# Kernel tuning notes

Measured on AMD Instinct MI355X. Metric: run time of the kernel, lower is better.

## Reference

```python
import jax, jax.numpy as jnp
import numpy as np

VOCAB, EMBED, HIDDEN = 256, 512, 1024
B, T = 64, 512


def setup_inputs() -> dict:
    key = jax.random.key(0)
    ks = jax.random.split(key, 12)
    s = 0.02
    return {
        "x": jax.random.randint(ks[0], (B, T), 0, VOCAB),
        "embed": jax.random.normal(ks[1], (VOCAB, EMBED), jnp.float32) * s,
        "Wih0": jax.random.normal(ks[2], (3 * HIDDEN, EMBED), jnp.float32) * s,
        "Whh0": jax.random.normal(ks[3], (3 * HIDDEN, HIDDEN), jnp.float32) * s,
        "bih0": jax.random.normal(ks[4], (3 * HIDDEN,), jnp.float32) * s,
        "bhh0": jax.random.normal(ks[5], (3 * HIDDEN,), jnp.float32) * s,
        "Wih1": jax.random.normal(ks[6], (3 * HIDDEN, HIDDEN), jnp.float32) * s,
        "Whh1": jax.random.normal(ks[7], (3 * HIDDEN, HIDDEN), jnp.float32) * s,
        "bih1": jax.random.normal(ks[8], (3 * HIDDEN,), jnp.float32) * s,
        "bhh1": jax.random.normal(ks[9], (3 * HIDDEN,), jnp.float32) * s,
        "W_out": jax.random.normal(ks[10], (VOCAB, HIDDEN), jnp.float32) * s,
        "b_out": jax.random.normal(ks[11], (VOCAB,), jnp.float32) * s,
    }


def gru_cell(inp, h, Wih, Whh, bih, bhh):
    # PyTorch GRUCell math.
    gi = inp @ Wih.T + bih  # (B, 3H)
    gh = h @ Whh.T + bhh    # (B, 3H)
    i_r, i_z, i_n = jnp.split(gi, 3, axis=-1)
    h_r, h_z, h_n = jnp.split(gh, 3, axis=-1)
    r = jax.nn.sigmoid(i_r + h_r)
    z = jax.nn.sigmoid(i_z + h_z)
    n = jnp.tanh(i_n + r * h_n)
    return (1.0 - z) * n + z * h


def reference(x, embed, Wih0, Whh0, bih0, bhh0, Wih1, Whh1, bih1, bhh1, W_out, b_out):
    emb = embed[x]                       # (B, T, E)
    xs = jnp.swapaxes(emb, 0, 1)         # (T, B, E)
    h0 = jnp.zeros((x.shape[0], HIDDEN), emb.dtype)

    def step(carry, inp_t):
        h_0, h_1 = carry
        h_0 = gru_cell(inp_t, h_0, Wih0, Whh0, bih0, bhh0)
        h_1 = gru_cell(h_0, h_1, Wih1, Whh1, bih1, bhh1)
        return (h_0, h_1), h_1

    _, outs = jax.lax.scan(step, (h0, h0), xs)   # outs: (T, B, H)
    outs = jnp.swapaxes(outs, 0, 1)              # (B, T, H)
    logits = outs @ W_out.T + b_out              # (B, T, V)
    return logits
```

## Files before the change

kernel.cpp:

```cpp
#include <hip/hip_runtime.h>
#include <stdint.h>

typedef short short8 __attribute__((ext_vector_type(8)));
typedef float f32x4 __attribute__((ext_vector_type(4)));
typedef unsigned short u16;

#define MFMA16(a, b, c) __builtin_amdgcn_mfma_f32_16x16x32_bf16((a), (b), (c), 0, 0, 0)

#define T_LEN 512
#define BATCH 64
#define EMB_D 512
#define HID 1024
#define VOC 256
#define NWG 128
#define RNN_THREADS 512

#define OFF_H0B   1048576u
#define OFF_H1B   1310720u
#define HB_ZERO_BYTES 524288u
#define OFF_EMB   1573120u
#define OFF_WIH0  (OFF_EMB + 33554432u)
#define OFF_WHH0  (OFF_WIH0 + 3145728u)
#define OFF_WIH1  (OFF_WHH0 + 6291456u)
#define OFF_WHH1  (OFF_WIH1 + 6291456u)
#define OFF_WOUT  (OFF_WHH1 + 6291456u)
#define OFF_H1ALL (OFF_WOUT + 524288u)
#define OFF_SYNC  (OFF_H1ALL + 67108864u)
#define SYNC_BYTES 16640u
#define WS_TOTAL  (OFF_SYNC + SYNC_BYTES)

static __device__ __forceinline__ u16 f2b(float f) {
  uint32_t u = __float_as_uint(f);
  u += 0x7FFFu + ((u >> 16) & 1u);
  return (u16)(u >> 16);
}
static __device__ __forceinline__ float sigm(float x) { return 1.0f / (1.0f + __expf(-x)); }

__global__ void cvt_kernel(const float* __restrict__ src, u16* __restrict__ dst, int n) {
  int i = ((int)blockIdx.x * 256 + (int)threadIdx.x) * 4;
  if (i + 4 <= n) {
    const float4 v = *(const float4*)(src + i);
    ushort4 o;
    o.x = f2b(v.x); o.y = f2b(v.y); o.z = f2b(v.z); o.w = f2b(v.w);
    *(ushort4*)(dst + i) = o;
  }
}

__global__ void emb_kernel(const int* __restrict__ x, const float* __restrict__ embed,
                           u16* __restrict__ emb_all) {
  const int r = (int)blockIdx.x * 4 + ((int)threadIdx.x >> 6);
  const int c = ((int)threadIdx.x & 63) * 8;
  const int t = r >> 6, b = r & 63;
  const int xi = x[b * T_LEN + t];
  const float* s = embed + (size_t)xi * EMB_D + c;
  const float4 v0 = *(const float4*)s;
  const float4 v1 = *(const float4*)(s + 4);
  ushort4 lo, hi;
  lo.x = f2b(v0.x); lo.y = f2b(v0.y); lo.z = f2b(v0.z); lo.w = f2b(v0.w);
  hi.x = f2b(v1.x); hi.y = f2b(v1.y); hi.z = f2b(v1.z); hi.w = f2b(v1.w);
  u16* d = emb_all + (size_t)r * EMB_D + c;
  *(ushort4*)d = lo;
  *(ushort4*)(d + 4) = hi;
}

__global__ __launch_bounds__(RNN_THREADS, 1) void rnn_persist_kernel(
    const u16* __restrict__ emb_all,
    const u16* __restrict__ A0i_r, const u16* __restrict__ A0i_z, const u16* __restrict__ A0i_n,
    const u16* __restrict__ A0h_r, const u16* __restrict__ A0h_z, const u16* __restrict__ A0h_n,
    const u16* __restrict__ A1i_r, const u16* __restrict__ A1i_z, const u16* __restrict__ A1i_n,
    const u16* __restrict__ A1h_r, const u16* __restrict__ A1h_z, const u16* __restrict__ A1h_n,
    const float* __restrict__ bih0, const float* __restrict__ bhh0,
    const float* __restrict__ bih1, const float* __restrict__ bhh1,
    u16* __restrict__ h0b, u16* __restrict__ h1b,
    u16* __restrict__ h1all, unsigned* __restrict__ flags)
{
  __shared__ __align__(16) float lds[16384];
  const int tid = (int)threadIdx.x;
  const int wv = tid >> 6;
  const int lane = tid & 63;
  const int lrow = lane & 15;
  const int lk8 = (lane >> 4) << 3;
  const int wgid = (int)blockIdx.x;
  const int layer = wgid >> 6;
  const int ubase = (wgid & 63) << 4;
  const bool iwave = (wv < 4);
  const bool l0i = (layer == 0) && iwave;

  const u16 *Ar, *Az, *An;
  int ldb, k0;
  if (layer == 0) {
    if (iwave) { Ar = A0i_r; Az = A0i_z; An = A0i_n; ldb = EMB_D; k0 = wv * 128; }
    else       { Ar = A0h_r; Az = A0h_z; An = A0h_n; ldb = HID;   k0 = (wv - 4) * 256; }
  } else {
    if (iwave) { Ar = A1i_r; Az = A1i_z; An = A1i_n; ldb = HID;   k0 = wv * 256; }
    else       { Ar = A1h_r; Az = A1h_z; An = A1h_n; ldb = HID;   k0 = (wv - 4) * 256; }
  }
  const size_t arow = (size_t)(ubase + lrow) * ldb;

  short8 a4R[4], a4Z[4], a4N[4];
  short8 a8R[8], a8Z[8], a8N[8];
  if (l0i) {
#pragma unroll
    for (int ks = 0; ks < 4; ++ks) {
      const int kk = k0 + ks * 32 + lk8;
      a4R[ks] = *(const short8*)(Ar + arow + kk);
      a4Z[ks] = *(const short8*)(Az + arow + kk);
      a4N[ks] = *(const short8*)(An + arow + kk);
    }
  } else {
#pragma unroll
    for (int ks = 0; ks < 8; ++ks) {
      const int kk = k0 + ks * 32 + lk8;
      a8R[ks] = *(const short8*)(Ar + arow + kk);
      a8Z[ks] = *(const short8*)(Az + arow + kk);
      a8N[ks] = *(const short8*)(An + arow + kk);
    }
  }

  const float* bi = layer ? bih1 : bih0;
  const float* bh = layer ? bhh1 : bhh0;
  const int eu = tid & 15;
  const int eug = ubase + eu;
  const float bR = bi[eug] + bh[eug];
  const float bZ = bi[HID + eug] + bh[HID + eug];
  const float bNi = bi[2 * HID + eug];
  const float bNh = bh[2 * HID + eug];
  const int el = ((eu >> 2) << 4);
  const int er = eu & 3;
  u16* hb = layer ? h1b : h0b;
  float hprev[2] = {0.f, 0.f};

  for (int s = 0; s <= T_LEN; ++s) {
    const bool active = (layer == 0) ? (s < T_LEN) : (s >= 1);
    if (active) {
      const int rdA = ((s + 1) & 1) * (BATCH * HID);
      const u16* Bp;
      if (layer == 0) Bp = iwave ? (emb_all + (size_t)s * (BATCH * EMB_D)) : (h0b + rdA);
      else            Bp = iwave ? (h0b + rdA) : (h1b + (s & 1) * (BATCH * HID));

      f32x4 acc0[4], acc1[4], accn[4];
#pragma unroll
      for (int bt = 0; bt < 4; ++bt) {
        acc0[bt] = (f32x4){0.f, 0.f, 0.f, 0.f};
        acc1[bt] = (f32x4){0.f, 0.f, 0.f, 0.f};
        accn[bt] = (f32x4){0.f, 0.f, 0.f, 0.f};
      }
      if (l0i) {
#pragma unroll
        for (int ks = 0; ks < 4; ++ks) {
          const int kk = k0 + ks * 32 + lk8;
#pragma unroll
          for (int bt = 0; bt < 4; ++bt) {
            const short8 bf = *(const short8*)(Bp + (size_t)(bt * 16 + lrow) * EMB_D + kk);
            acc0[bt] = MFMA16(a4R[ks], bf, acc0[bt]);
            acc1[bt] = MFMA16(a4Z[ks], bf, acc1[bt]);
            accn[bt] = MFMA16(a4N[ks], bf, accn[bt]);
          }
        }
      } else {
#pragma unroll
        for (int ks = 0; ks < 8; ++ks) {
          const int kk = k0 + ks * 32 + lk8;
#pragma unroll
          for (int bt = 0; bt < 4; ++bt) {
            const short8 bf = *(const short8*)(Bp + (size_t)(bt * 16 + lrow) * HID + kk);
            acc0[bt] = MFMA16(a8R[ks], bf, acc0[bt]);
            acc1[bt] = MFMA16(a8Z[ks], bf, acc1[bt]);
            accn[bt] = MFMA16(a8N[ks], bf, accn[bt]);
          }
        }
      }
      if (iwave) {
#pragma unroll
        for (int bt = 0; bt < 4; ++bt)
#pragma unroll
          for (int r = 0; r < 4; ++r) {
            const int ix = lane ^ (r << 3);
            lds[(((wv * 4 + 0) * 4 + bt) * 256) + r * 64 + ix] = acc0[bt][r];
            lds[(((wv * 4 + 1) * 4 + bt) * 256) + r * 64 + ix] = acc1[bt][r];
            lds[(((wv * 4 + 2) * 4 + bt) * 256) + r * 64 + ix] = accn[bt][r];
          }
      }
      __syncthreads();
      if (!iwave) {
        const int z = wv - 4;
#pragma unroll
        for (int bt = 0; bt < 4; ++bt)
#pragma unroll
          for (int r = 0; r < 4; ++r) {
            const int ix = lane ^ (r << 3);
            float* p0 = &lds[(((z * 4 + 0) * 4 + bt) * 256) + r * 64 + ix];
            float* p1 = &lds[(((z * 4 + 1) * 4 + bt) * 256) + r * 64 + ix];
            *p0 = *p0 + acc0[bt][r];
            *p1 = *p1 + acc1[bt][r];
            lds[(((z * 4 + 3) * 4 + bt) * 256) + r * 64 + ix] = accn[bt][r];
          }
      }
      __syncthreads();
      {
        const int wrt = (layer == 0) ? (s & 1) * (BATCH * HID) : ((s + 1) & 1) * (BATCH * HID);
#pragma unroll
        for (int pp = 0; pp < 2; ++pp) {
          const int p = tid + pp * RNN_THREADS;
          const int b = (p >> 4) & 63;
          const int l = el | (b & 15);
          const int bt = b >> 4;
          const int ix = l ^ (er << 3);
          float sr = 0.f, sz = 0.f, sni = 0.f, snh = 0.f;
#pragma unroll
          for (int z = 0; z < 4; ++z) {
            sr  += lds[(((z * 4 + 0) * 4 + bt) * 256) + er * 64 + ix];
            sz  += lds[(((z * 4 + 1) * 4 + bt) * 256) + er * 64 + ix];
            sni += lds[(((z * 4 + 2) * 4 + bt) * 256) + er * 64 + ix];
            snh += lds[(((z * 4 + 3) * 4 + bt) * 256) + er * 64 + ix];
          }
          const float rg = sigm(sr + bR);
          const float zg = sigm(sz + bZ);
          const float ng = tanhf(sni + bNi + rg * (snh + bNh));
          const float hn = (1.0f - zg) * ng + zg * hprev[pp];
          hprev[pp] = hn;
          const u16 hv = f2b(hn);
          hb[wrt + b * HID + eug] = hv;
          if (layer) h1all[((size_t)(s - 1) * BATCH + b) * HID + eug] = hv;
        }
      }
    }
    if (s < T_LEN) {
      __syncthreads();
      const unsigned ep = (unsigned)(s + 1);
      if (tid == 0)
        __hip_atomic_store(&flags[wgid * 32], ep, __ATOMIC_RELEASE, __HIP_MEMORY_SCOPE_AGENT);
      if (tid < NWG) {
        while (__hip_atomic_load(&flags[tid * 32], __ATOMIC_ACQUIRE,
                                 __HIP_MEMORY_SCOPE_AGENT) < ep)
          __builtin_amdgcn_s_sleep(1);
      }
      __syncthreads();
    }
  }
}

__global__ __launch_bounds__(256, 2) void logits_kernel(
    const u16* __restrict__ h1all, const u16* __restrict__ Woutb,
    const float* __restrict__ bout, float* __restrict__ out)
{
  __shared__ __align__(16) short lds[16 * 4 * 64 * 8];
  const int tid = (int)threadIdx.x;
  const int wv = tid >> 6, lane = tid & 63;
  const int lrow = lane & 15, lk8 = (lane >> 4) << 3;
  const int row0 = (int)blockIdx.x * 64 + wv * 16;
  f32x4 acc[16];
#pragma unroll
  for (int i = 0; i < 16; ++i) acc[i] = (f32x4){0.f, 0.f, 0.f, 0.f};

  for (int kc = 0; kc < HID; kc += 128) {
    __syncthreads();
#pragma unroll
    for (int j = 0; j < 16; ++j) {
      const int slot = tid + j * 256;
      const int ct = slot >> 8, kt = (slot >> 6) & 3, l = slot & 63;
      *(short8*)&lds[slot * 8] =
          *(const short8*)(Woutb + (size_t)(ct * 16 + (l & 15)) * HID + kc + kt * 32 + ((l >> 4) << 3));
    }
    __syncthreads();
#pragma unroll
    for (int kt = 0; kt < 4; ++kt) {
      const short8 af = *(const short8*)(h1all + (size_t)(row0 + lrow) * HID + kc + kt * 32 + lk8);
#pragma unroll
      for (int ct = 0; ct < 16; ++ct) {
        const short8 bf = *(const short8*)&lds[((ct * 4 + kt) * 64 + lane) * 8];
        acc[ct] = MFMA16(af, bf, acc[ct]);
      }
    }
  }
#pragma unroll
  for (int ct = 0; ct < 16; ++ct) {
    const int v = ct * 16 + lrow;
    const float bo = bout[v];
#pragma unroll
    for (int r = 0; r < 4; ++r) {
      const int row = row0 + (lane >> 4) * 4 + r;
      const int t = row >> 6, b = row & 63;
      out[((size_t)(b * T_LEN + t)) * VOC + v] = acc[ct][r] + bo;
    }
  }
}

extern "C" void kernel_launch(void* const* d_in, const int* in_sizes, int n_in,
                              void* d_out, int out_size, void* d_ws, size_t ws_size,
                              hipStream_t stream) {
  const int*   x     = (const int*)d_in[0];
  const float* embed = (const float*)d_in[1];
  const float* Wih0  = (const float*)d_in[2];
  const float* Whh0  = (const float*)d_in[3];
  const float* bih0  = (const float*)d_in[4];
  const float* bhh0  = (const float*)d_in[5];
  const float* Wih1  = (const float*)d_in[6];
  const float* Whh1  = (const float*)d_in[7];
  const float* bih1  = (const float*)d_in[8];
  const float* bhh1  = (const float*)d_in[9];
  const float* Wout  = (const float*)d_in[10];
  const float* bout  = (const float*)d_in[11];
  float* out = (float*)d_out;
  char* ws = (char*)d_ws;
  if (ws_size < (size_t)WS_TOTAL) return;

  hipMemsetAsync(ws + OFF_H0B, 0, HB_ZERO_BYTES, stream);
  hipMemsetAsync(ws + OFF_SYNC, 0, SYNC_BYTES, stream);
  cvt_kernel<<<1536, 256, 0, stream>>>(Wih0, (u16*)(ws + OFF_WIH0), 3072 * 512);
  cvt_kernel<<<3072, 256, 0, stream>>>(Whh0, (u16*)(ws + OFF_WHH0), 3072 * 1024);
  cvt_kernel<<<3072, 256, 0, stream>>>(Wih1, (u16*)(ws + OFF_WIH1), 3072 * 1024);
  cvt_kernel<<<3072, 256, 0, stream>>>(Whh1, (u16*)(ws + OFF_WHH1), 3072 * 1024);
  cvt_kernel<<<256, 256, 0, stream>>>(Wout, (u16*)(ws + OFF_WOUT), 256 * 1024);
  emb_kernel<<<8192, 256, 0, stream>>>(x, embed, (u16*)(ws + OFF_EMB));

  const u16* wih0b = (const u16*)(ws + OFF_WIH0);
  const u16* whh0b = (const u16*)(ws + OFF_WHH0);
  const u16* wih1b = (const u16*)(ws + OFF_WIH1);
  const u16* whh1b = (const u16*)(ws + OFF_WHH1);

  rnn_persist_kernel<<<NWG, RNN_THREADS, 0, stream>>>(
      (const u16*)(ws + OFF_EMB),
      wih0b, wih0b + 524288, wih0b + 1048576,
      whh0b, whh0b + 1048576, whh0b + 2097152,
      wih1b, wih1b + 1048576, wih1b + 2097152,
      whh1b, whh1b + 1048576, whh1b + 2097152,
      bih0, bhh0, bih1, bhh1,
      (u16*)(ws + OFF_H0B), (u16*)(ws + OFF_H1B),
      (u16*)(ws + OFF_H1ALL), (unsigned*)(ws + OFF_SYNC));

  logits_kernel<<<512, 256, 0, stream>>>((const u16*)(ws + OFF_H1ALL),
                                         (const u16*)(ws + OFF_WOUT), bout, out);
}
```

Before: 8.112 ms.

## Use relaxed coherent loads/stores instead of acquire-release grid barrier fences

Replaces the release/acquire atomics in the per-step grid barrier with relaxed ones. Cross-workgroup hidden-state traffic now uses agent-scope atomic stores and 64-bit atomic loads, plus an explicit vmcnt wait, so the barrier no longer triggers full cache writeback and invalidate fences. It also stops keeping the weight fragments resident in registers: they are reloaded from global memory every step, which frees VGPRs but adds load traffic. The elementwise stage now handles two adjacent units per thread with packed 32-bit stores. Correctness depends on the relaxed atomics plus the waitcnt actually providing the cross-CU ordering that the fences used to give.

After: 11.59 ms. +42.9%, slower.

```diff
diff --git a/kernel.cpp b/kernel.cpp
--- a/kernel.cpp
+++ b/kernel.cpp
@@ -4,6 +4,7 @@
 typedef short short8 __attribute__((ext_vector_type(8)));
 typedef float f32x4 __attribute__((ext_vector_type(4)));
 typedef unsigned short u16;
+typedef unsigned long long u64;
 
 #define MFMA16(a, b, c) __builtin_amdgcn_mfma_f32_16x16x32_bf16((a), (b), (c), 0, 0, 0)
 
@@ -35,6 +36,13 @@
   return (u16)(u >> 16);
 }
 static __device__ __forceinline__ float sigm(float x) { return 1.0f / (1.0f + __expf(-x)); }
+
+static __device__ __forceinline__ short8 loadB_coh(const u16* p) {
+  union { u64 q[2]; short8 v; } u;
+  u.q[0] = __hip_atomic_load((u64*)p,       __ATOMIC_RELAXED, __HIP_MEMORY_SCOPE_AGENT);
+  u.q[1] = __hip_atomic_load((u64*)(p + 4), __ATOMIC_RELAXED, __HIP_MEMORY_SCOPE_AGENT);
+  return u.v;
+}
 
 __global__ void cvt_kernel(const float* __restrict__ src, u16* __restrict__ dst, int n) {
   int i = ((int)blockIdx.x * 256 + (int)threadIdx.x) * 4;
@@ -97,38 +105,25 @@
   }
   const size_t arow = (size_t)(ubase + lrow) * ldb;
 
-  short8 a4R[4], a4Z[4], a4N[4];
-  short8 a8R[8], a8Z[8], a8N[8];
-  if (l0i) {
-#pragma unroll
-    for (int ks = 0; ks < 4; ++ks) {
-      const int kk = k0 + ks * 32 + lk8;
-      a4R[ks] = *(const short8*)(Ar + arow + kk);
-      a4Z[ks] = *(const short8*)(Az + arow + kk);
-      a4N[ks] = *(const short8*)(An + arow + kk);
-    }
-  } else {
-#pragma unroll
-    for (int ks = 0; ks < 8; ++ks) {
-      const int kk = k0 + ks * 32 + lk8;
-      a8R[ks] = *(const short8*)(Ar + arow + kk);
-      a8Z[ks] = *(const short8*)(Az + arow + kk);
-      a8N[ks] = *(const short8*)(An + arow + kk);
-    }
-  }
-
   const float* bi = layer ? bih1 : bih0;
   const float* bh = layer ? bhh1 : bhh0;
-  const int eu = tid & 15;
-  const int eug = ubase + eu;
-  const float bR = bi[eug] + bh[eug];
-  const float bZ = bi[HID + eug] + bh[HID + eug];
-  const float bNi = bi[2 * HID + eug];
-  const float bNh = bh[2 * HID + eug];
-  const int el = ((eu >> 2) << 4);
-  const int er = eu & 3;
+  const int u0 = (tid & 7) * 2;
+  const int eb = tid >> 3;
+  const int eug0 = ubase + u0, eug1 = eug0 + 1;
+  const float bR0 = bi[eug0] + bh[eug0];
+  const float bZ0 = bi[HID + eug0] + bh[HID + eug0];
+  const float bNi0 = bi[2 * HID + eug0];
+  const float bNh0 = bh[2 * HID + eug0];
+  const float bR1 = bi[eug1] + bh[eug1];
+  const float bZ1 = bi[HID + eug1] + bh[HID + eug1];
+  const float bNi1 = bi[2 * HID + eug1];
+  const float bNh1 = bh[2 * HID + eug1];
+  const int l_e = ((u0 >> 2) << 4) | (eb & 15);
+  const int r0 = u0 & 3, r1 = r0 + 1;
+  const int ebt = eb >> 4;
+  const int ix0 = l_e ^ (r0 << 3), ix1 = l_e ^ (r1 << 3);
   u16* hb = layer ? h1b : h0b;
-  float hprev[2] = {0.f, 0.f};
+  float hp0 = 0.f, hp1 = 0.f;
 
   for (int s = 0; s <= T_LEN; ++s) {
     const bool active = (layer == 0) ? (s < T_LEN) : (s >= 1);
@@ -149,24 +144,30 @@
 #pragma unroll
         for (int ks = 0; ks < 4; ++ks) {
           const int kk = k0 + ks * 32 + lk8;
+          const short8 ar = *(const short8*)(Ar + arow + kk);
+          const short8 az = *(const short8*)(Az + arow + kk);
+          const short8 an = *(const short8*)(An + arow + kk);
 #pragma unroll
           for (int bt = 0; bt < 4; ++bt) {
             const short8 bf = *(const short8*)(Bp + (size_t)(bt * 16 + lrow) * EMB_D + kk);
-            acc0[bt] = MFMA16(a4R[ks], bf, acc0[bt]);
-            acc1[bt] = MFMA16(a4Z[ks], bf, acc1[bt]);
-            accn[bt] = MFMA16(a4N[ks], bf, accn[bt]);
+            acc0[bt] = MFMA16(ar, bf, acc0[bt]);
+            acc1[bt] = MFMA16(az, bf, acc1[bt]);
+            accn[bt] = MFMA16(an, bf, accn[bt]);
           }
         }
       } else {
 #pragma unroll
         for (int ks = 0; ks < 8; ++ks) {
           const int kk = k0 + ks * 32 + lk8;
+          const short8 ar = *(const short8*)(Ar + arow + kk);
+          const short8 az = *(const short8*)(Az + arow + kk);
+          const short8 an = *(const short8*)(An + arow + kk);
 #pragma unroll
           for (int bt = 0; bt < 4; ++bt) {
-            const short8 bf = *(const short8*)(Bp + (size_t)(bt * 16 + lrow) * HID + kk);
-            acc0[bt] = MFMA16(a8R[ks], bf, acc0[bt]);
-            acc1[bt] = MFMA16(a8Z[ks], bf, acc1[bt]);
-            accn[bt] = MFMA16(a8N[ks], bf, accn[bt]);
+            const short8 bf = loadB_coh(Bp + (size_t)(bt * 16 + lrow) * HID + kk);
+            acc0[bt] = MFMA16(ar, bf, acc0[bt]);
+            acc1[bt] = MFMA16(az, bf, acc1[bt]);
+            accn[bt] = MFMA16(an, bf, accn[bt]);
           }
         }
       }
@@ -199,42 +200,47 @@
       __syncthreads();
       {
         const int wrt = (layer == 0) ? (s & 1) * (BATCH * HID) : ((s + 1) & 1) * (BATCH * HID);
-#pragma unroll
-        for (int pp = 0; pp < 2; ++pp) {
-          const int p = tid + pp * RNN_THREADS;
-          const int b = (p >> 4) & 63;
-          const int l = el | (b & 15);
-          const int bt = b >> 4;
-          const int ix = l ^ (er << 3);
-          float sr = 0.f, sz = 0.f, sni = 0.f, snh = 0.f;
-#pragma unroll
-          for (int z = 0; z < 4; ++z) {
-            sr  += lds[(((z * 4 + 0) * 4 + bt) * 256) + er * 64 + ix];
-            sz  += lds[(((z * 4 + 1) * 4 + bt) * 256) + er * 64 + ix];
-            sni += lds[(((z * 4 + 2) * 4 + bt) * 256) + er * 64 + ix];
-            snh += lds[(((z * 4 + 3) * 4 + bt) * 256) + er * 64 + ix];
-          }
-          const float rg = sigm(sr + bR);
-          const float zg = sigm(sz + bZ);
-          const float ng = tanhf(sni + bNi + rg * (snh + bNh));
-          const float hn = (1.0f - zg) * ng + zg * hprev[pp];
-          hprev[pp] = hn;
-          const u16 hv = f2b(hn);
-          hb[wrt + b * HID + eug] = hv;
-          if (layer) h1all[((size_t)(s - 1) * BATCH + b) * HID + eug] = hv;
+        float sr0 = 0.f, sz0 = 0.f, sni0 = 0.f, snh0 = 0.f;
+        float sr1 = 0.f, sz1 = 0.f, sni1 = 0.f, snh1 = 0.f;
+#pragma unroll
+        for (int z = 0; z < 4; ++z) {
+          sr0  += lds[(((z * 4 + 0) * 4 + ebt) * 256) + r0 * 64 + ix0];
+          sz0  += lds[(((z * 4 + 1) * 4 + ebt) * 256) + r0 * 64 + ix0];
+          sni0 += lds[(((z * 4 + 2) * 4 + ebt) * 256) + r0 * 64 + ix0];
+          snh0 += lds[(((z * 4 + 3) * 4 + ebt) * 256) + r0 * 64 + ix0];
+          sr1  += lds[(((z * 4 + 0) * 4 + ebt) * 256) + r1 * 64 + ix1];
+          sz1  += lds[(((z * 4 + 1) * 4 + ebt) * 256) + r1 * 64 + ix1];
+          sni1 += lds[(((z * 4 + 2) * 4 + ebt) * 256) + r1 * 64 + ix1];
+          snh1 += lds[(((z * 4 + 3) * 4 + ebt) * 256) + r1 * 64 + ix1];
         }
+        const float rg0 = sigm(sr0 + bR0);
+        const float zg0 = sigm(sz0 + bZ0);
+        const float ng0 = tanhf(sni0 + bNi0 + rg0 * (snh0 + bNh0));
+        const float hn0 = (1.0f - zg0) * ng0 + zg0 * hp0;
+        const float rg1 = sigm(sr1 + bR1);
+        const float zg1 = sigm(sz1 + bZ1);
+        const float ng1 = tanhf(sni1 + bNi1 + rg1 * (snh1 + bNh1));
+        const float hn1 = (1.0f - zg1) * ng1 + zg1 * hp1;
+        hp0 = hn0; hp1 = hn1;
+        const unsigned packed = (unsigned)f2b(hn0) | ((unsigned)f2b(hn1) << 16);
+        __hip_atomic_store((unsigned*)&hb[wrt + eb * HID + eug0], packed,
+                           __ATOMIC_RELAXED, __HIP_MEMORY_SCOPE_AGENT);
+        if (layer)
+          *(unsigned*)&h1all[((size_t)(s - 1) * BATCH + eb) * HID + eug0] = packed;
       }
     }
     if (s < T_LEN) {
+      asm volatile("s_waitcnt vmcnt(0)" ::: "memory");
       __syncthreads();
       const unsigned ep = (unsigned)(s + 1);
       if (tid == 0)
-        __hip_atomic_store(&flags[wgid * 32], ep, __ATOMIC_RELEASE, __HIP_MEMORY_SCOPE_AGENT);
+        __hip_atomic_store(&flags[wgid * 32], ep, __ATOMIC_RELAXED, __HIP_MEMORY_SCOPE_AGENT);
       if (tid < NWG) {
-        while (__hip_atomic_load(&flags[tid * 32], __ATOMIC_ACQUIRE,
+        while (__hip_atomic_load(&flags[tid * 32], __ATOMIC_RELAXED,
                                  __HIP_MEMORY_SCOPE_AGENT) < ep)
           __builtin_amdgcn_s_sleep(1);
       }
+      asm volatile("" ::: "memory");
       __syncthreads();
     }
   }
```
